# Kernel tuning notes

Measured on AMD Instinct MI355X. Metric: run time of the kernel, lower is better.

The kernel has to match this reference:

```python
import jax, jax.numpy as jnp
import numpy as np

D_IN = 2048
D_OUT = 2048
NUM_HEADS = 16
HEAD_DIM = D_OUT // NUM_HEADS


def setup_inputs() -> dict:
    key = jax.random.key(0)
    ks = jax.random.split(key, 6)
    scale = 1.0 / np.sqrt(D_IN)
    x = jax.random.normal(ks[0], (4, 2048, D_IN), dtype=jnp.float32)
    # Linear weights stored [out, in] like torch; applied as x @ W.T
    W_query = jax.random.normal(ks[1], (D_OUT, D_IN), dtype=jnp.float32) * scale
    W_key = jax.random.normal(ks[2], (D_OUT, D_IN), dtype=jnp.float32) * scale
    W_value = jax.random.normal(ks[3], (D_OUT, D_IN), dtype=jnp.float32) * scale
    W_out = jax.random.normal(ks[4], (D_OUT, D_OUT), dtype=jnp.float32) * (1.0 / np.sqrt(D_OUT))
    b_out = jax.random.normal(ks[5], (D_OUT,), dtype=jnp.float32) * 0.01
    return {"x": x, "W_query": W_query, "W_key": W_key, "W_value": W_value,
            "W_out": W_out, "b_out": b_out}


def reference(x, W_query, W_key, W_value, W_out, b_out):
    b, t, _ = x.shape
    # projections (torch Linear: x @ W.T), no qkv bias
    q = jnp.einsum('btd,od->bto', x, W_query)
    k = jnp.einsum('btd,od->bto', x, W_key)
    v = jnp.einsum('btd,od->bto', x, W_value)
    # split heads: [b, nh, t, hd]
    q = q.reshape(b, t, NUM_HEADS, HEAD_DIM).transpose(0, 2, 1, 3)
    k = k.reshape(b, t, NUM_HEADS, HEAD_DIM).transpose(0, 2, 1, 3)
    v = v.reshape(b, t, NUM_HEADS, HEAD_DIM).transpose(0, 2, 1, 3)
    # attention scores [b, nh, t, t], causal mask (strict upper triangle -> -inf)
    scores = jnp.einsum('bhqd,bhkd->bhqk', q, k)
    causal = jnp.triu(jnp.ones((t, t), dtype=bool), k=1)
    scores = jnp.where(causal, -jnp.inf, scores)
    attn = jax.nn.softmax(scores / np.sqrt(HEAD_DIM), axis=-1)
    # dropout p=0.0 -> identity
    ctx = jnp.einsum('bhqk,bhkd->bhqd', attn, v)
    ctx = ctx.transpose(0, 2, 1, 3).reshape(b, t, D_OUT)
    return jnp.einsum('btd,od->bto', ctx, W_out) + b_out
```

## Files before the change

### kernel.cpp

```cpp
#include <hip/hip_runtime.h>
#include <hip/hip_bf16.h>
#include <cstdint>
#include <cstddef>

typedef __bf16 bf16_t;
typedef __bf16 bf16x8 __attribute__((ext_vector_type(8)));
typedef float floatx4 __attribute__((ext_vector_type(4)));

#define BATCH 4
#define SEQ   2048
#define DMODEL 2048
#define NHEADS 16
#define HDIM  128
#define MTOK  (BATCH * SEQ)

__device__ __forceinline__ void gload_lds16(const bf16_t* g, bf16_t* l) {
  __builtin_amdgcn_global_load_lds(
      (const __attribute__((address_space(1))) void*)g,
      (__attribute__((address_space(3))) void*)l, 16, 0, 0);
}

__global__ void detect_dtype(const unsigned* __restrict__ x, int* __restrict__ flag) {
  __shared__ int cnt[256];
  const int t = threadIdx.x;
  int c = 0;
  for (int i = 0; i < 8; i++) {
    unsigned w = x[t * 8 + i];
    unsigned e = (w >> 7) & 0xFFu;
    c += (e >= 100u && e <= 140u) ? 1 : 0;
  }
  cnt[t] = c;
  __syncthreads();
  for (int s = 128; s > 0; s >>= 1) {
    if (t < s) cnt[t] += cnt[t + s];
    __syncthreads();
  }
  if (t == 0) *flag = (cnt[0] > 1433) ? 1 : 0;
}

__device__ __forceinline__ bf16x8 cvt8(const float* __restrict__ p) {
  float4 a = *(const float4*)p;
  float4 b = *(const float4*)(p + 4);
  bf16x8 o;
  o[0] = (bf16_t)a.x; o[1] = (bf16_t)a.y; o[2] = (bf16_t)a.z; o[3] = (bf16_t)a.w;
  o[4] = (bf16_t)b.x; o[5] = (bf16_t)b.y; o[6] = (bf16_t)b.z; o[7] = (bf16_t)b.w;
  return o;
}

__global__ void convert_to_bf16(const void* __restrict__ src, bf16_t* __restrict__ dst,
                                int n, const int* __restrict__ flag) {
  const int i = (blockIdx.x * blockDim.x + threadIdx.x) * 8;
  if (i >= n) return;
  if (*flag) *(bf16x8*)(dst + i) = *(const bf16x8*)((const bf16_t*)src + i);
  else       *(bf16x8*)(dst + i) = cvt8((const float*)src + i);
}

template<bool BIAS, bool A_ST, bool B_ST, bool OUT_DYN>
__global__ __launch_bounds__(256, 2)
void gemm_bt(const void* __restrict__ Av, const void* __restrict__ Bv,
             const void* __restrict__ biasv, void* __restrict__ Cv,
             int M, int N, int K, const int* __restrict__ flag, float scale) {
  const bool isbf = (*flag != 0);
  __shared__ alignas(16) bf16_t sA[128 * 32];
  __shared__ alignas(16) bf16_t sB[128 * 32];
  const int tid  = threadIdx.x;
  const int lane = tid & 63;
  const int wave = tid >> 6;
  const int wm = wave >> 1, wn = wave & 1;
  const int m0 = blockIdx.y * 128;
  const int n0 = blockIdx.x * 128;
  const int q4  = lane >> 4;
  const int l16 = lane & 15;

  floatx4 acc[4][4] = {};

  for (int k0 = 0; k0 < K; k0 += 32) {
    __syncthreads();
    #pragma unroll
    for (int j = 0; j < 2; ++j) {
      const int c = (wave * 2 + j) * 64 + lane;
      const int row = c >> 2, kp = c & 3;
      const size_t aoff = (size_t)(m0 + row) * K + (k0 + kp * 8);
      if (A_ST) {
        gload_lds16((const bf16_t*)Av + aoff, sA + (wave * 2 + j) * 512);
      } else {
        bf16x8 v = isbf ? *(const bf16x8*)((const bf16_t*)Av + aoff)
                        : cvt8((const float*)Av + aoff);
        *(bf16x8*)(sA + c * 8) = v;
      }
      const size_t boff = (size_t)(n0 + row) * K + (k0 + kp * 8);
      if (B_ST) {
        gload_lds16((const bf16_t*)Bv + boff, sB + (wave * 2 + j) * 512);
      } else {
        bf16x8 v = isbf ? *(const bf16x8*)((const bf16_t*)Bv + boff)
                        : cvt8((const float*)Bv + boff);
        *(bf16x8*)(sB + c * 8) = v;
      }
    }
    __syncthreads();

    bf16x8 af[4], bf[4];
    #pragma unroll
    for (int i = 0; i < 4; i++)
      af[i] = *(const bf16x8*)(sA + (wm * 64 + i * 16 + l16) * 32 + q4 * 8);
    #pragma unroll
    for (int i = 0; i < 4; i++)
      bf[i] = *(const bf16x8*)(sB + (wn * 64 + i * 16 + l16) * 32 + q4 * 8);
    #pragma unroll
    for (int i = 0; i < 4; i++)
      #pragma unroll
      for (int jn = 0; jn < 4; jn++)
        acc[i][jn] = __builtin_amdgcn_mfma_f32_16x16x32_bf16(af[i], bf[jn], acc[i][jn], 0, 0, 0);
  }

  #pragma unroll
  for (int i = 0; i < 4; i++) {
    const int mrow = m0 + wm * 64 + i * 16 + q4 * 4;
    #pragma unroll
    for (int jn = 0; jn < 4; jn++) {
      const int ncol = n0 + wn * 64 + jn * 16 + l16;
      float badd = 0.0f;
      if (BIAS)
        badd = (float)((const bf16_t*)biasv)[ncol];
      #pragma unroll
      for (int r = 0; r < 4; r++) {
        const size_t idx = (size_t)(mrow + r) * N + ncol;
        const float val = acc[i][jn][r] * scale + badd;
        if (OUT_DYN && !isbf) ((float*)Cv)[idx] = val;
        else                  ((bf16_t*)Cv)[idx] = (bf16_t)val;
      }
    }
  }
}

__global__ __launch_bounds__(256, 2)
void attn_fused(const bf16_t* __restrict__ Qb, const bf16_t* __restrict__ Kb,
                const bf16_t* __restrict__ VTb, bf16_t* __restrict__ ctx) {
  __shared__ alignas(16) bf16_t sK[2][32 * 128];
  __shared__ alignas(16) bf16_t sVT[2][128 * 32];
  __shared__ alignas(16) bf16_t sP[4 * 32 * 40];

  const int tid = threadIdx.x, lane = tid & 63, wave = tid >> 6;
  const int q4 = lane >> 4, l16 = lane & 15;
  const int h  = blockIdx.y;
  const int b  = blockIdx.z;
  const size_t qkbase = (size_t)b * SEQ * DMODEL + (size_t)h * HDIM;
  const size_t vtbase = (size_t)(h * HDIM) * MTOK + (size_t)b * SEQ;
  bf16_t* sPw = sP + wave * 1280;

  auto STAGE = [&](int kt, int bs) {
    const int kb = kt * 32;
    #pragma unroll
    for (int j = 0; j < 2; ++j) {
      const int c = (wave * 2 + j) * 64 + lane;
      const int row = c >> 4;
      const int gg = (c & 15) ^ (row & 15);
      gload_lds16(Kb + qkbase + (size_t)(kb + row) * DMODEL + gg * 8,
                  sK[bs] + (wave * 2 + j) * 512);
    }
    #pragma unroll
    for (int j = 0; j < 2; ++j) {
      const int c = (wave * 2 + j) * 64 + lane;
      const int row = c >> 2, g = c & 3;
      gload_lds16(VTb + vtbase + (size_t)row * MTOK + (kb + g * 8),
                  sVT[bs] + (wave * 2 + j) * 512);
    }
  };

  #pragma unroll 1
  for (int pass = 0; pass < 2; ++pass) {
    const int tile = pass ? (int)blockIdx.x : (15 - (int)blockIdx.x);
    const int q0 = tile * 128;
    const int qw = q0 + wave * 32;

    bf16x8 qf[2][4];
    #pragma unroll
    for (int mb = 0; mb < 2; mb++) {
      const bf16_t* qp = Qb + qkbase + (size_t)(qw + mb * 16 + l16) * DMODEL + q4 * 8;
      #pragma unroll
      for (int kc = 0; kc < 4; kc++) qf[mb][kc] = *(const bf16x8*)(qp + kc * 32);
    }

    floatx4 o[2][8] = {};
    float rs[2][4] = {};
    const int ntiles = q0 / 32 + 4;

    STAGE(0, 0);
    __syncthreads();

    for (int kt = 0; kt < ntiles; ++kt) {
      const int cur = kt & 1;
      if (kt + 1 < ntiles) STAGE(kt + 1, cur ^ 1);
      const int kb = kt * 32;

      if (kb < qw + 32) {
        floatx4 s[2][2] = {};
        #pragma unroll
        for (int kc = 0; kc < 4; kc++) {
          const int sw = (kc * 4 + q4) ^ l16;
          bf16x8 kf0 = *(const bf16x8*)(sK[cur] + ((l16)      * 16 + sw) * 8);
          bf16x8 kf1 = *(const bf16x8*)(sK[cur] + ((16 + l16) * 16 + sw) * 8);
          #pragma unroll
          for (int mb = 0; mb < 2; mb++) {
            s[mb][0] = __builtin_amdgcn_mfma_f32_16x16x32_bf16(qf[mb][kc], kf0, s[mb][0], 0, 0, 0);
            s[mb][1] = __builtin_amdgcn_mfma_f32_16x16x32_bf16(qf[mb][kc], kf1, s[mb][1], 0, 0, 0);
          }
        }

        if (kb + 31 > qw) {
          #pragma unroll
          for (int mb = 0; mb < 2; mb++)
            #pragma unroll
            for (int cc = 0; cc < 2; cc++) {
              const int col = kb + cc * 16 + l16;
              #pragma unroll
              for (int r = 0; r < 4; r++)
                if (col > qw + mb * 16 + q4 * 4 + r) s[mb][cc][r] = -1e30f;
            }
        }

        #pragma unroll
        for (int mb = 0; mb < 2; mb++)
          #pragma unroll
          for (int cc = 0; cc < 2; cc++)
            #pragma unroll
            for (int r = 0; r < 4; r++) {
              const float p = __builtin_amdgcn_exp2f(s[mb][cc][r]);
              rs[mb][r] += p;
              sPw[(mb * 16 + q4 * 4 + r) * 40 + cc * 16 + l16] = (bf16_t)p;
            }

        bf16x8 pf[2];
        #pragma unroll
        for (int mb = 0; mb < 2; mb++)
          pf[mb] = *(const bf16x8*)(sPw + (mb * 16 + l16) * 40 + q4 * 8);
        #pragma unroll
        for (int db = 0; db < 8; db++) {
          bf16x8 vf = *(const bf16x8*)(sVT[cur] + (db * 16 + l16) * 32 + q4 * 8);
          #pragma unroll
          for (int mb = 0; mb < 2; mb++)
            o[mb][db] = __builtin_amdgcn_mfma_f32_16x16x32_bf16(pf[mb], vf, o[mb][db], 0, 0, 0);
        }
      }

      __syncthreads();
    }

    #pragma unroll
    for (int mb = 0; mb < 2; mb++)
      #pragma unroll
      for (int r = 0; r < 4; r++) {
        #pragma unroll
        for (int d = 1; d < 16; d <<= 1) rs[mb][r] += __shfl_xor(rs[mb][r], d);
        rs[mb][r] = 1.0f / rs[mb][r];
      }

    #pragma unroll
    for (int mb = 0; mb < 2; mb++)
      #pragma unroll
      for (int db = 0; db < 8; db++)
        #pragma unroll
        for (int r = 0; r < 4; r++) {
          const int qrow = qw + mb * 16 + q4 * 4 + r;
          ctx[qkbase + (size_t)qrow * DMODEL + db * 16 + l16] =
              (bf16_t)(o[mb][db][r] * rs[mb][r]);
        }
  }
}

extern "C" void kernel_launch(void* const* d_in, const int* in_sizes, int n_in,
                              void* d_out, int out_size, void* d_ws, size_t ws_size,
                              hipStream_t stream) {
  const size_t szX = (size_t)MTOK * DMODEL;
  const size_t szW = (size_t)DMODEL * DMODEL;

  char* ws = (char*)d_ws;
  int*    flag = (int*)ws;       ws += 256;
  bf16_t* xb   = (bf16_t*)ws;    ws += szX * 2;
  bf16_t* Q    = (bf16_t*)ws;    ws += szX * 2;
  bf16_t* K_   = (bf16_t*)ws;    ws += szX * 2;
  bf16_t* VT   = (bf16_t*)ws;    ws += szX * 2;
  bf16_t* ctx  = xb;

  bf16_t* Wq_b   = VT;
  bf16_t* Wk_b   = VT + szW;
  bf16_t* Wv_b   = (bf16_t*)d_out;
  bf16_t* Wout_b = K_;
  bf16_t* bias_b = K_ + szW;

  const float kC = 0.08838834764831845f * 1.4426950408889634f;

  detect_dtype<<<1, 256, 0, stream>>>((const unsigned*)d_in[0], flag);
  convert_to_bf16<<<(int)(szX / 8 / 256), 256, 0, stream>>>(d_in[0], xb,   (int)szX, flag);
  convert_to_bf16<<<(int)(szW / 8 / 256), 256, 0, stream>>>(d_in[1], Wq_b, (int)szW, flag);
  convert_to_bf16<<<(int)(szW / 8 / 256), 256, 0, stream>>>(d_in[2], Wk_b, (int)szW, flag);
  convert_to_bf16<<<(int)(szW / 8 / 256), 256, 0, stream>>>(d_in[3], Wv_b, (int)szW, flag);

  dim3 blk(256);
  dim3 gg(DMODEL / 128, MTOK / 128);
  gemm_bt<false, true, true, false><<<gg, blk, 0, stream>>>(xb, Wq_b, nullptr, Q,  MTOK, DMODEL, DMODEL, flag, kC);
  gemm_bt<false, true, true, false><<<gg, blk, 0, stream>>>(xb, Wk_b, nullptr, K_, MTOK, DMODEL, DMODEL, flag, 1.0f);
  dim3 gv(MTOK / 128, DMODEL / 128);
  gemm_bt<false, true, true, false><<<gv, blk, 0, stream>>>(Wv_b, xb, nullptr, VT, DMODEL, MTOK, DMODEL, flag, 1.0f);

  dim3 ga(SEQ / 256, NHEADS, BATCH);
  attn_fused<<<ga, blk, 0, stream>>>(Q, K_, VT, ctx);

  convert_to_bf16<<<(int)(szW / 8 / 256), 256, 0, stream>>>(d_in[4], Wout_b, (int)szW, flag);
  convert_to_bf16<<<1, 256, 0, stream>>>(d_in[5], bias_b, DMODEL, flag);
  gemm_bt<true, true, true, true><<<gg, blk, 0, stream>>>(ctx, Wout_b, bias_b, d_out, MTOK, DMODEL, DMODEL, flag, 1.0f);
}
```

Before: 603.3 us.

## Replace 128x128 GEMM with 256x256 double-buffered, pipelined 8-wave kernel

Swaps the simple 128x128-tile GEMM, which synchronised twice per 32-wide k-step, for a 256x256-tile kernel with 512 threads. It stages 64-wide k tiles split into two halves in double-buffered LDS, issues async global-to-LDS loads for future stages between MFMA phases, and uses s_waitcnt counts, raw barriers and setprio. The goal is more reuse per byte loaded and load latency hidden behind MFMA work across the four projection GEMMs. The cost is 128KB of LDS per block, which may limit occupancy to one block despite launch_bounds(512,2), and fragile hand-coded vmcnt accounting.

```diff
diff --git a/kernel.cpp b/kernel.cpp
--- a/kernel.cpp
+++ b/kernel.cpp
@@ -18,6 +18,12 @@
   __builtin_amdgcn_global_load_lds(
       (const __attribute__((address_space(1))) void*)g,
       (__attribute__((address_space(3))) void*)l, 16, 0, 0);
+}
+
+__device__ __forceinline__ void wg_barrier() {
+  asm volatile("" ::: "memory");
+  __builtin_amdgcn_s_barrier();
+  asm volatile("" ::: "memory");
 }
 
 __global__ void detect_dtype(const unsigned* __restrict__ x, int* __restrict__ flag) {
@@ -55,77 +61,129 @@
   else       *(bf16x8*)(dst + i) = cvt8((const float*)src + i);
 }
 
-template<bool BIAS, bool A_ST, bool B_ST, bool OUT_DYN>
-__global__ __launch_bounds__(256, 2)
-void gemm_bt(const void* __restrict__ Av, const void* __restrict__ Bv,
-             const void* __restrict__ biasv, void* __restrict__ Cv,
+template<bool BIAS, bool OUT_DYN>
+__global__ __launch_bounds__(512, 2)
+void gemm256(const bf16_t* __restrict__ A, const bf16_t* __restrict__ B,
+             const bf16_t* __restrict__ biasv, void* __restrict__ Cv,
              int M, int N, int K, const int* __restrict__ flag, float scale) {
   const bool isbf = (*flag != 0);
-  __shared__ alignas(16) bf16_t sA[128 * 32];
-  __shared__ alignas(16) bf16_t sB[128 * 32];
+  __shared__ alignas(16) bf16_t sA[2][2][256 * 32];
+  __shared__ alignas(16) bf16_t sB[2][2][256 * 32];
   const int tid  = threadIdx.x;
   const int lane = tid & 63;
   const int wave = tid >> 6;
-  const int wm = wave >> 1, wn = wave & 1;
-  const int m0 = blockIdx.y * 128;
-  const int n0 = blockIdx.x * 128;
-  const int q4  = lane >> 4;
-  const int l16 = lane & 15;
-
-  floatx4 acc[4][4] = {};
-
-  for (int k0 = 0; k0 < K; k0 += 32) {
-    __syncthreads();
+  const int wm = wave >> 2, wn = wave & 3;
+  const int q4 = lane >> 4, l16 = lane & 15;
+  const int m0 = blockIdx.y * 256;
+  const int n0 = blockIdx.x * 256;
+  const int NT = K >> 6;
+
+  auto STG = [&](const bf16_t* __restrict__ G, int grow0, bf16_t* slot, int kt, int kh) {
     #pragma unroll
     for (int j = 0; j < 2; ++j) {
       const int c = (wave * 2 + j) * 64 + lane;
-      const int row = c >> 2, kp = c & 3;
-      const size_t aoff = (size_t)(m0 + row) * K + (k0 + kp * 8);
-      if (A_ST) {
-        gload_lds16((const bf16_t*)Av + aoff, sA + (wave * 2 + j) * 512);
-      } else {
-        bf16x8 v = isbf ? *(const bf16x8*)((const bf16_t*)Av + aoff)
-                        : cvt8((const float*)Av + aoff);
-        *(bf16x8*)(sA + c * 8) = v;
-      }
-      const size_t boff = (size_t)(n0 + row) * K + (k0 + kp * 8);
-      if (B_ST) {
-        gload_lds16((const bf16_t*)Bv + boff, sB + (wave * 2 + j) * 512);
-      } else {
-        bf16x8 v = isbf ? *(const bf16x8*)((const bf16_t*)Bv + boff)
-                        : cvt8((const float*)Bv + boff);
-        *(bf16x8*)(sB + c * 8) = v;
-      }
-    }
-    __syncthreads();
-
-    bf16x8 af[4], bf[4];
-    #pragma unroll
-    for (int i = 0; i < 4; i++)
-      af[i] = *(const bf16x8*)(sA + (wm * 64 + i * 16 + l16) * 32 + q4 * 8);
-    #pragma unroll
-    for (int i = 0; i < 4; i++)
-      bf[i] = *(const bf16x8*)(sB + (wn * 64 + i * 16 + l16) * 32 + q4 * 8);
-    #pragma unroll
-    for (int i = 0; i < 4; i++)
-      #pragma unroll
-      for (int jn = 0; jn < 4; jn++)
-        acc[i][jn] = __builtin_amdgcn_mfma_f32_16x16x32_bf16(af[i], bf[jn], acc[i][jn], 0, 0, 0);
+      const int row = c >> 2, c8 = c & 3;
+      gload_lds16(G + (size_t)(grow0 + row) * K + (kt * 64 + kh * 32 + c8 * 8),
+                  slot + (wave * 2 + j) * 512);
+    }
+  };
+
+  floatx4 acc[8][4] = {};
+
+  const int aoff = (wm * 128 + l16) * 32 + q4 * 8;
+  const int boff = (wn * 64  + l16) * 32 + q4 * 8;
+
+  STG(A, m0, &sA[0][0][0], 0, 0);
+  STG(B, n0, &sB[0][0][0], 0, 0);
+  STG(A, m0, &sA[0][1][0], 0, 1);
+  STG(B, n0, &sB[0][1][0], 0, 1);
+  STG(A, m0, &sA[1][0][0], 1, 0);
+  STG(B, n0, &sB[1][0][0], 1, 0);
+  asm volatile("s_waitcnt vmcnt(8)" ::: "memory");
+  wg_barrier();
+
+  #pragma unroll 2
+  for (int kt = 0; kt < NT; ++kt) {
+    const int buf = kt & 1;
+    const bf16_t* sA0 = &sA[buf][0][0];
+    const bf16_t* sA1 = &sA[buf][1][0];
+    const bf16_t* sB0 = &sB[buf][0][0];
+    const bf16_t* sB1 = &sB[buf][1][0];
+    bf16x8 af[4], bfr[4];
+
+    #pragma unroll
+    for (int mf = 0; mf < 4; mf++) af[mf]  = *(const bf16x8*)(sA0 + aoff + mf * 512);
+    #pragma unroll
+    for (int nf = 0; nf < 4; nf++) bfr[nf] = *(const bf16x8*)(sB0 + boff + nf * 512);
+    if (kt + 1 < NT) STG(A, m0, &sA[buf ^ 1][1][0], kt + 1, 1);
+    wg_barrier();
+    __builtin_amdgcn_s_setprio(1);
+    #pragma unroll
+    for (int mf = 0; mf < 4; mf++)
+      #pragma unroll
+      for (int nf = 0; nf < 4; nf++)
+        acc[mf][nf] = __builtin_amdgcn_mfma_f32_16x16x32_bf16(af[mf], bfr[nf], acc[mf][nf], 0, 0, 0);
+    __builtin_amdgcn_s_setprio(0);
+    wg_barrier();
+
+    #pragma unroll
+    for (int mf = 0; mf < 4; mf++) af[mf] = *(const bf16x8*)(sA0 + aoff + (64 * 32) + mf * 512);
+    if (kt + 1 < NT) STG(B, n0, &sB[buf ^ 1][1][0], kt + 1, 1);
+    wg_barrier();
+    __builtin_amdgcn_s_setprio(1);
+    #pragma unroll
+    for (int mf = 0; mf < 4; mf++)
+      #pragma unroll
+      for (int nf = 0; nf < 4; nf++)
+        acc[4 + mf][nf] = __builtin_amdgcn_mfma_f32_16x16x32_bf16(af[mf], bfr[nf], acc[4 + mf][nf], 0, 0, 0);
+    __builtin_amdgcn_s_setprio(0);
+    if (kt < NT - 1) asm volatile("s_waitcnt vmcnt(8)" ::: "memory");
+    else             asm volatile("s_waitcnt vmcnt(0)" ::: "memory");
+    wg_barrier();
+
+    #pragma unroll
+    for (int mf = 0; mf < 4; mf++) af[mf]  = *(const bf16x8*)(sA1 + aoff + mf * 512);
+    #pragma unroll
+    for (int nf = 0; nf < 4; nf++) bfr[nf] = *(const bf16x8*)(sB1 + boff + nf * 512);
+    if (kt + 2 < NT) STG(A, m0, &sA[buf][0][0], kt + 2, 0);
+    wg_barrier();
+    __builtin_amdgcn_s_setprio(1);
+    #pragma unroll
+    for (int mf = 0; mf < 4; mf++)
+      #pragma unroll
+      for (int nf = 0; nf < 4; nf++)
+        acc[mf][nf] = __builtin_amdgcn_mfma_f32_16x16x32_bf16(af[mf], bfr[nf], acc[mf][nf], 0, 0, 0);
+    __builtin_amdgcn_s_setprio(0);
+    wg_barrier();
+
+    #pragma unroll
+    for (int mf = 0; mf < 4; mf++) af[mf] = *(const bf16x8*)(sA1 + aoff + (64 * 32) + mf * 512);
+    if (kt + 2 < NT) STG(B, n0, &sB[buf][0][0], kt + 2, 0);
+    wg_barrier();
+    __builtin_amdgcn_s_setprio(1);
+    #pragma unroll
+    for (int mf = 0; mf < 4; mf++)
+      #pragma unroll
+      for (int nf = 0; nf < 4; nf++)
+        acc[4 + mf][nf] = __builtin_amdgcn_mfma_f32_16x16x32_bf16(af[mf], bfr[nf], acc[4 + mf][nf], 0, 0, 0);
+    __builtin_amdgcn_s_setprio(0);
+    if (kt < NT - 2)       asm volatile("s_waitcnt vmcnt(8)" ::: "memory");
+    else if (kt == NT - 2) asm volatile("s_waitcnt vmcnt(4)" ::: "memory");
+    wg_barrier();
   }
 
   #pragma unroll
-  for (int i = 0; i < 4; i++) {
-    const int mrow = m0 + wm * 64 + i * 16 + q4 * 4;
-    #pragma unroll
-    for (int jn = 0; jn < 4; jn++) {
-      const int ncol = n0 + wn * 64 + jn * 16 + l16;
+  for (int mf = 0; mf < 8; mf++) {
+    const int mrow = m0 + wm * 128 + mf * 16 + q4 * 4;
+    #pragma unroll
+    for (int nf = 0; nf < 4; nf++) {
+      const int ncol = n0 + wn * 64 + nf * 16 + l16;
       float badd = 0.0f;
-      if (BIAS)
-        badd = (float)((const bf16_t*)biasv)[ncol];
+      if (BIAS) badd = (float)biasv[ncol];
       #pragma unroll
       for (int r = 0; r < 4; r++) {
         const size_t idx = (size_t)(mrow + r) * N + ncol;
-        const float val = acc[i][jn][r] * scale + badd;
+        const float val = acc[mf][nf][r] * scale + badd;
         if (OUT_DYN && !isbf) ((float*)Cv)[idx] = val;
         else                  ((bf16_t*)Cv)[idx] = (bf16_t)val;
       }
@@ -296,17 +354,17 @@
   convert_to_bf16<<<(int)(szW / 8 / 256), 256, 0, stream>>>(d_in[2], Wk_b, (int)szW, flag);
   convert_to_bf16<<<(int)(szW / 8 / 256), 256, 0, stream>>>(d_in[3], Wv_b, (int)szW, flag);
 
-  dim3 blk(256);
-  dim3 gg(DMODEL / 128, MTOK / 128);
-  gemm_bt<false, true, true, false><<<gg, blk, 0, stream>>>(xb, Wq_b, nullptr, Q,  MTOK, DMODEL, DMODEL, flag, kC);
-  gemm_bt<false, true, true, false><<<gg, blk, 0, stream>>>(xb, Wk_b, nullptr, K_, MTOK, DMODEL, DMODEL, flag, 1.0f);
-  dim3 gv(MTOK / 128, DMODEL / 128);
-  gemm_bt<false, true, true, false><<<gv, blk, 0, stream>>>(Wv_b, xb, nullptr, VT, DMODEL, MTOK, DMODEL, flag, 1.0f);
+  dim3 blk(512);
+  dim3 gg(DMODEL / 256, MTOK / 256);
+  gemm256<false, false><<<gg, blk, 0, stream>>>(xb, Wq_b, nullptr, Q,  MTOK, DMODEL, DMODEL, flag, kC);
+  gemm256<false, false><<<gg, blk, 0, stream>>>(xb, Wk_b, nullptr, K_, MTOK, DMODEL, DMODEL, flag, 1.0f);
+  dim3 gv(MTOK / 256, DMODEL / 256);
+  gemm256<false, false><<<gv, blk, 0, stream>>>(Wv_b, xb, nullptr, VT, DMODEL, MTOK, DMODEL, flag, 1.0f);
 
   dim3 ga(SEQ / 256, NHEADS, BATCH);
-  attn_fused<<<ga, blk, 0, stream>>>(Q, K_, VT, ctx);
+  attn_fused<<<ga, dim3(256), 0, stream>>>(Q, K_, VT, ctx);
 
   convert_to_bf16<<<(int)(szW / 8 / 256), 256, 0, stream>>>(d_in[4], Wout_b, (int)szW, flag);
   convert_to_bf16<<<1, 256, 0, stream>>>(d_in[5], bias_b, DMODEL, flag);
-  gemm_bt<true, true, true, true><<<gg, blk, 0, stream>>>(ctx, Wout_b, bias_b, d_out, MTOK, DMODEL, DMODEL, flag, 1.0f);
-}
+  gemm256<true, true><<<gg, blk, 0, stream>>>(ctx, Wout_b, bias_b, d_out, MTOK, DMODEL, DMODEL, flag, 1.0f);
+}
```

New measurement: 573.3 us. 1.05x faster.
